# Optimization experiments

Measured on AMD Instinct MI355X. Metric: run time of the kernel, lower is better.

The kernel has to match this reference:

```python
import jax, jax.numpy as jnp
import numpy as np

B, C, H, W = 8, 512, 128, 128
WS = 8

def _proj(x, w, b):
    # 1x1 conv == channel GEMM: (B,C,H,W) x (Cout,Cin) -> (B,Cout,H,W)
    return jnp.einsum('bchw,oc->bohw', x, w) + b[None, :, None, None]

def _split_windows(x):
    # (B,C,H,W) -> (B*nH*nW, ws*ws, C)
    b, c, h, w = x.shape
    x = x.reshape(b, c, h // WS, WS, w // WS, WS)
    x = x.transpose(0, 2, 4, 3, 5, 1)
    return x.reshape(-1, WS * WS, c)

def _merge_windows(x, b, c, h, w):
    # (B*nH*nW, ws*ws, C) -> (B,C,H,W)
    x = x.reshape(b, h // WS, w // WS, WS, WS, c)
    x = x.transpose(0, 5, 1, 3, 2, 4)
    return x.reshape(b, c, h, w)

def setup_inputs() -> dict:
    key = jax.random.key(0)
    ks = jax.random.split(key, 9)
    s = 1.0 / np.sqrt(C)
    return {
        'x': jax.random.normal(ks[0], (B, C, H, W), jnp.float32),
        'wq': jax.random.normal(ks[1], (C, C), jnp.float32) * s,
        'bq': jnp.zeros((C,), jnp.float32),
        'wk': jax.random.normal(ks[2], (C, C), jnp.float32) * s,
        'bk': jnp.zeros((C,), jnp.float32),
        'wv': jax.random.normal(ks[3], (C, C), jnp.float32) * s,
        'bv': jnp.zeros((C,), jnp.float32),
        'wo': jax.random.normal(ks[4], (C, C), jnp.float32) * s,
        'bo': jnp.zeros((C,), jnp.float32),
    }

def reference(x, wq, bq, wk, bk, wv, bv, wo, bo):
    b, c, h, w = x.shape
    q = _split_windows(_proj(x, wq, bq))  # (nWin, ws*ws, C)
    k = _split_windows(_proj(x, wk, bk))
    v = _split_windows(_proj(x, wv, bv))
    attn = jnp.einsum('nqc,nkc->nqk', q, k) / jnp.sqrt(jnp.asarray(c, x.dtype))
    attn = jax.nn.softmax(attn, axis=-1)
    out = jnp.einsum('nqk,nkc->nqc', attn, v)
    out = _merge_windows(out, b, c, h, w)
    return _proj(out, wo, bo)
```

## Files before the change

### kernel.cpp

```cpp
#include <hip/hip_runtime.h>

typedef __attribute__((ext_vector_type(8))) short bf16x8;
typedef __attribute__((ext_vector_type(4))) float f32x4;

#define MFMA16(a, b, c) __builtin_amdgcn_mfma_f32_16x16x32_bf16((a), (b), (c), 0, 0, 0)

__device__ __forceinline__ float b2f(unsigned short u) {
  unsigned int v = ((unsigned int)u) << 16;
  return __builtin_bit_cast(float, v);
}
__device__ __forceinline__ unsigned short f2b(float f) {
  unsigned int u = __builtin_bit_cast(unsigned int, f);
  u += 0x7fffu + ((u >> 16) & 1u);
  return (unsigned short)(u >> 16);
}
__device__ __forceinline__ void gload16(const void* g, void* l) {
  __builtin_amdgcn_global_load_lds(
      (const __attribute__((address_space(1))) unsigned int*)g,
      (__attribute__((address_space(3))) unsigned int*)l, 16, 0, 0);
}

__global__ __launch_bounds__(256) void k_wconv(
    const float* __restrict__ src, unsigned short* __restrict__ dst) {
  const int i = (blockIdx.x * 256 + threadIdx.x) * 4;
  const float4 v = *(const float4*)(src + i);
  uint2 p;
  p.x = (unsigned int)f2b(v.x) | ((unsigned int)f2b(v.y) << 16);
  p.y = (unsigned int)f2b(v.z) | ((unsigned int)f2b(v.w) << 16);
  *(uint2*)(dst + i) = p;
}

__global__ __launch_bounds__(256) void k_wtrans(
    const float* __restrict__ in, unsigned short* __restrict__ out) {
  __shared__ unsigned short tile[64][72];
  const int r0 = blockIdx.x << 6, s0 = blockIdx.y << 6;
  const int t = threadIdx.x;
  {
    const int sl = t >> 3, rl = (t & 7) << 3;
#pragma unroll
    for (int pass = 0; pass < 2; ++pass) {
      const int s = sl + pass * 32;
      const float* src = in + (size_t)(s0 + s) * 512 + r0 + rl;
      const float4 f0 = ((const float4*)src)[0];
      const float4 f1 = ((const float4*)src)[1];
      tile[rl + 0][s] = f2b(f0.x);
      tile[rl + 1][s] = f2b(f0.y);
      tile[rl + 2][s] = f2b(f0.z);
      tile[rl + 3][s] = f2b(f0.w);
      tile[rl + 4][s] = f2b(f1.x);
      tile[rl + 5][s] = f2b(f1.y);
      tile[rl + 6][s] = f2b(f1.z);
      tile[rl + 7][s] = f2b(f1.w);
    }
  }
  __syncthreads();
  {
    const int rl = t >> 3, sl = (t & 7) << 3;
#pragma unroll
    for (int pass = 0; pass < 2; ++pass) {
      const int r = rl + pass * 32;
      uint4 v = *(const uint4*)&tile[r][sl];
      *(uint4*)(out + (size_t)(r0 + r) * 512 + s0 + sl) = v;
    }
  }
}

__global__ __launch_bounds__(256) void k_bvo(
    const float* __restrict__ wo, const float* __restrict__ bv,
    const float* __restrict__ bo, float* __restrict__ bvo) {
  const int o = blockIdx.x * 256 + threadIdx.x;
  float acc = bo[o];
  const float* row = wo + (size_t)o * 512;
  for (int j = 0; j < 512; ++j) acc += row[j] * bv[j];
  bvo[o] = acc;
}

__global__ __launch_bounds__(256) void k_ub(
    const float* __restrict__ wk, const float* __restrict__ bq,
    float* __restrict__ u) {
  const int c = blockIdx.x * 256 + threadIdx.x;
  float acc = 0.f;
  for (int o = 0; o < 512; ++o) acc += bq[o] * wk[(size_t)o * 512 + c];
  u[c] = acc;
}

__global__ __launch_bounds__(256) void k_transpose(
    const float* __restrict__ X, unsigned short* __restrict__ XT,
    unsigned short* __restrict__ XV) {
  const int bx = blockIdx.x;
  const int wt = bx & 1, ht = bx >> 1;
  const int c0 = blockIdx.y << 5;
  const int b = blockIdx.z;
  const int w0 = wt << 6, h0 = ht << 3;
  const int t = threadIdx.x;
  const int cg = t & 3, pg = t >> 2;
  const int wi = pg >> 3, hh = pg & 7;
  const int h = h0 + hh, w = w0 + wi * 8;
  const int cbase = c0 + cg * 8;

  const float* xsrc = X + (size_t)b * 8388608u + (size_t)cbase * 16384 +
                      (size_t)h * 128 + w;
  float f[8][8];
#pragma unroll
  for (int ci = 0; ci < 8; ++ci) {
    const float4 a0 = ((const float4*)(xsrc + (size_t)ci * 16384))[0];
    const float4 a1 = ((const float4*)(xsrc + (size_t)ci * 16384))[1];
    f[ci][0] = a0.x; f[ci][1] = a0.y; f[ci][2] = a0.z; f[ci][3] = a0.w;
    f[ci][4] = a1.x; f[ci][5] = a1.y; f[ci][6] = a1.z; f[ci][7] = a1.w;
  }

  unsigned short* xtdst =
      XT + (size_t)b * 8388608u + ((size_t)h * 128 + w) * 512 + cbase;
#pragma unroll
  for (int pi = 0; pi < 8; ++pi) {
    unsigned short o[8];
#pragma unroll
    for (int ci = 0; ci < 8; ++ci) o[ci] = f2b(f[ci][pi]);
    *(uint4*)(xtdst + (size_t)pi * 512) = *(const uint4*)o;
  }

  const int win = b * 256 + ht * 16 + wt * 8 + wi;
  unsigned short* xvdst =
      XV + (size_t)cbase * 131072 + (size_t)win * 64 + hh * 8;
#pragma unroll
  for (int ci = 0; ci < 8; ++ci) {
    unsigned short o[8];
#pragma unroll
    for (int pi = 0; pi < 8; ++pi) o[pi] = f2b(f[ci][pi]);
    *(uint4*)(xvdst + (size_t)ci * 131072) = *(const uint4*)o;
  }
}

template <int MODE>
__global__ __launch_bounds__(512, 2) void k_gemm256(
    const unsigned short* __restrict__ A, const unsigned short* __restrict__ B,
    const float* __restrict__ bias0, void* __restrict__ C0v) {
  __shared__ unsigned short lsA[4][256 * 32];
  __shared__ unsigned short lsB[4][256 * 32];
  const int bid = blockIdx.x;
  int mt, nt;
  if (MODE == 0) {
    const int work = ((bid & 7) << 7) + (bid >> 3);
    mt = work >> 1; nt = work & 1;
  } else if (MODE == 2) {
    const int work = ((bid & 7) << 7) + (bid >> 3);
    nt = work >> 1; mt = work & 1;
  } else {
    mt = bid & 1; nt = bid >> 1;
  }
  const int m0 = mt << 8, n0 = nt << 8;

  const int t = threadIdx.x;
  const int l = t & 63;
  const int lr = l & 15, lg = l >> 4;
  const int w = t >> 6;
  const int wr = w >> 2, wc = w & 3;
  const int ra = wr << 7, rb = wc << 6;
  const int srowS = t >> 2;
  const int scolS = (t & 3) << 3;

  f32x4 acc[8][4];
#pragma unroll
  for (int i = 0; i < 8; ++i)
#pragma unroll
    for (int j = 0; j < 4; ++j) acc[i][j] = f32x4{0.f, 0.f, 0.f, 0.f};

  auto stage = [&](int kt) {
    const int buf = kt & 3, k0 = kt << 5;
#pragma unroll
    for (int hh = 0; hh < 2; ++hh) {
      gload16(A + (size_t)(m0 + srowS + hh * 128) * 512 + k0 + scolS,
              &lsA[buf][(srowS + hh * 128) * 32 + scolS]);
      gload16(B + (size_t)(n0 + srowS + hh * 128) * 512 + k0 + scolS,
              &lsB[buf][(srowS + hh * 128) * 32 + scolS]);
    }
  };
  auto compute = [&](int kt) {
    const int buf = kt & 3;
    bf16x8 af[8], bfv[4];
#pragma unroll
    for (int i = 0; i < 8; ++i)
      af[i] = *(const bf16x8*)&lsA[buf][(ra + i * 16 + lr) * 32 + lg * 8];
#pragma unroll
    for (int j = 0; j < 4; ++j)
      bfv[j] = *(const bf16x8*)&lsB[buf][(rb + j * 16 + lr) * 32 + lg * 8];
    __builtin_amdgcn_s_setprio(1);
#pragma unroll
    for (int i = 0; i < 8; ++i)
#pragma unroll
      for (int j = 0; j < 4; ++j)
        acc[i][j] = MFMA16(af[i], bfv[j], acc[i][j]);
    __builtin_amdgcn_s_setprio(0);
  };

  stage(0); stage(1); stage(2);

#define GITER(kt, vm)                                        \
  asm volatile("s_waitcnt vmcnt(" #vm ")" ::: "memory");     \
  __builtin_amdgcn_s_barrier();                              \
  __builtin_amdgcn_sched_barrier(0);                         \
  if ((kt) + 3 < 16) stage((kt) + 3);                        \
  compute(kt);                                               \
  __builtin_amdgcn_sched_barrier(0);                         \
  __builtin_amdgcn_s_barrier();

  GITER(0, 8)  GITER(1, 8)  GITER(2, 8)  GITER(3, 8)
  GITER(4, 8)  GITER(5, 8)  GITER(6, 8)  GITER(7, 8)
  GITER(8, 8)  GITER(9, 8)  GITER(10, 8) GITER(11, 8)
  GITER(12, 8) GITER(13, 8) GITER(14, 4) GITER(15, 0)
#undef GITER

#pragma unroll
  for (int i = 0; i < 8; ++i) {
    const int cmb = m0 + ra + i * 16 + lg * 4;
#pragma unroll
    for (int j = 0; j < 4; ++j) {
      const int cn = n0 + rb + j * 16 + lr;
      const float bn = (MODE == 0) ? bias0[cn] : 0.f;
#pragma unroll
      for (int r = 0; r < 4; ++r) {
        const int cm = cmb + r;
        if (MODE == 0) {
          ((unsigned short*)C0v)[(size_t)cm * 512 + cn] = f2b(acc[i][j][r] + bn);
        } else if (MODE == 2) {
          const float val = acc[i][j][r] + bias0[cm];
          const int bb = cn >> 14, p = cn & 16383;
          ((float*)C0v)[(size_t)bb * 8388608 + (size_t)cm * 16384 + p] = val;
        } else {
          ((unsigned short*)C0v)[(size_t)cm * 512 + cn] = f2b(acc[i][j][r]);
        }
      }
    }
  }
}

__global__ __launch_bounds__(256) void k_attn(
    const unsigned short* __restrict__ Q, const unsigned short* __restrict__ XT,
    const unsigned short* __restrict__ XV, unsigned short* __restrict__ Y) {
  __shared__ unsigned short P_lds[4][64][72];
  const int t = threadIdx.x, w = t >> 6, l = t & 63;
  const int lr = l & 15, lg = l >> 4;
  const int grp = ((blockIdx.x & 7) << 6) + (blockIdx.x >> 3);
  const int win = grp * 4 + w;
  const int b = win >> 8, th = (win >> 4) & 15, tw = win & 15;
  const size_t p_base = (size_t)b * 16384 + (size_t)th * 1024 + (size_t)tw * 8;
  const size_t rowpix = p_base + (size_t)(lr >> 3) * 128 + (lr & 7);
  const unsigned short* qbase = Q + rowpix * 512;
  const unsigned short* kbase = XT + rowpix * 512;

  f32x4 acc[4][4];
#pragma unroll
  for (int i = 0; i < 4; ++i)
#pragma unroll
    for (int j = 0; j < 4; ++j) acc[i][j] = f32x4{0.f, 0.f, 0.f, 0.f};

  bf16x8 kp[2][4], qp[2][4];
#pragma unroll
  for (int pp = 0; pp < 2; ++pp) {
    const int co = pp * 32 + lg * 8;
#pragma unroll
    for (int i = 0; i < 4; ++i) {
      kp[pp][i] = *(const bf16x8*)(kbase + (size_t)i * 131072 + co);
      qp[pp][i] = *(const bf16x8*)(qbase + (size_t)i * 131072 + co);
    }
  }
#pragma unroll
  for (int cs = 0; cs < 16; ++cs) {
    const int cb = cs & 1;
    __builtin_amdgcn_s_setprio(1);
#pragma unroll
    for (int mt = 0; mt < 4; ++mt)
#pragma unroll
      for (int qt = 0; qt < 4; ++qt)
        acc[mt][qt] = MFMA16(kp[cb][mt], qp[cb][qt], acc[mt][qt]);
    __builtin_amdgcn_s_setprio(0);
    if (cs + 2 < 16) {
      const int co = (cs + 2) * 32 + lg * 8;
#pragma unroll
      for (int i = 0; i < 4; ++i) {
        kp[cb][i] = *(const bf16x8*)(kbase + (size_t)i * 131072 + co);
        qp[cb][i] = *(const bf16x8*)(qbase + (size_t)i * 131072 + co);
      }
    }
  }

  const float scale = 0.044194173824159216f;
#pragma unroll
  for (int qt = 0; qt < 4; ++qt) {
    float pv[4][4];
    float mx = -3.0e38f;
#pragma unroll
    for (int mt = 0; mt < 4; ++mt)
#pragma unroll
      for (int j = 0; j < 4; ++j) {
        const float s = acc[mt][qt][j] * scale;
        pv[mt][j] = s;
        mx = fmaxf(mx, s);
      }
    mx = fmaxf(mx, __shfl_xor(mx, 16));
    mx = fmaxf(mx, __shfl_xor(mx, 32));
    float sum = 0.f;
#pragma unroll
    for (int mt = 0; mt < 4; ++mt)
#pragma unroll
      for (int j = 0; j < 4; ++j) {
        const float e = __expf(pv[mt][j] - mx);
        pv[mt][j] = e;
        sum += e;
      }
    sum += __shfl_xor(sum, 16);
    sum += __shfl_xor(sum, 32);
    const float inv = 1.f / sum;
#pragma unroll
    for (int mt = 0; mt < 4; ++mt)
#pragma unroll
      for (int j = 0; j < 4; j += 2) {
        const unsigned int pk =
            (unsigned int)f2b(pv[mt][j] * inv) |
            ((unsigned int)f2b(pv[mt][j + 1] * inv) << 16);
        *(unsigned int*)&P_lds[w][qt * 16 + lr][mt * 16 + lg * 4 + j] = pk;
      }
  }

  bf16x8 pa0[4], pa1[4];
#pragma unroll
  for (int qt = 0; qt < 4; ++qt) {
    pa0[qt] = *(const bf16x8*)&P_lds[w][qt * 16 + lr][lg * 8];
    pa1[qt] = *(const bf16x8*)&P_lds[w][qt * 16 + lr][32 + lg * 8];
  }
  const unsigned short* vbase =
      XV + (size_t)lr * 131072 + (size_t)win * 64 + lg * 8;
  unsigned short* ystore =
      Y + (p_base + (size_t)(lg >> 1) * 128 + ((lg & 1) << 2)) * 512 + lr;

  bf16x8 v0p[2], v1p[2];
#pragma unroll
  for (int pp = 0; pp < 2; ++pp) {
    const unsigned short* vp = vbase + (size_t)pp * (16 * 131072);
    v0p[pp] = *(const bf16x8*)vp;
    v1p[pp] = *(const bf16x8*)(vp + 32);
  }
#pragma unroll
  for (int nt = 0; nt < 32; ++nt) {
    const int cb = nt & 1;
    f32x4 o[4];
    __builtin_amdgcn_s_setprio(1);
#pragma unroll
    for (int qt = 0; qt < 4; ++qt) {
      o[qt] = f32x4{0.f, 0.f, 0.f, 0.f};
      o[qt] = MFMA16(pa0[qt], v0p[cb], o[qt]);
      o[qt] = MFMA16(pa1[qt], v1p[cb], o[qt]);
    }
    __builtin_amdgcn_s_setprio(0);
    if (nt + 2 < 32) {
      const unsigned short* vp = vbase + (size_t)(nt + 2) * (16 * 131072);
      v0p[cb] = *(const bf16x8*)vp;
      v1p[cb] = *(const bf16x8*)(vp + 32);
    }
#pragma unroll
    for (int qt = 0; qt < 4; ++qt)
#pragma unroll
      for (int r = 0; r < 4; ++r)
        ystore[(size_t)qt * 131072 + r * 512 + nt * 16] = f2b(o[qt][r]);
  }
}

extern "C" void kernel_launch(void* const* d_in, const int* in_sizes, int n_in,
                              void* d_out, int out_size, void* d_ws,
                              size_t ws_size, hipStream_t stream) {
  (void)in_sizes; (void)n_in; (void)out_size;
  const float* x = (const float*)d_in[0];
  const float* wq = (const float*)d_in[1];
  const float* bq = (const float*)d_in[2];
  const float* wk = (const float*)d_in[3];
  const float* bk = (const float*)d_in[4];
  const float* wv = (const float*)d_in[5];
  const float* bv = (const float*)d_in[6];
  const float* wo = (const float*)d_in[7];
  const float* bo = (const float*)d_in[8];
  (void)bk;

  const size_t NEED = (size_t)(2097152 + 3 * 67108864) * 2;
  if (ws_size < NEED) return;

  unsigned short* wb = (unsigned short*)d_ws;
  unsigned short* wqT = wb;
  unsigned short* wkT = wb + 262144;
  unsigned short* wvT = wb + 524288;
  unsigned short* wo_b = wb + 786432;
  unsigned short* wvo = wb + 1048576;
  float* bvo = (float*)(wb + 1310720);
  float* ub = (float*)(wb + 1311744);
  unsigned short* Bqk = wb + 1572864;
  unsigned short* xT = wb + 2097152;
  unsigned short* xV = xT + 67108864;
  unsigned short* Ybuf = xV + 67108864;
  unsigned short* Tq = (unsigned short*)d_out;

  k_wtrans<<<dim3(8, 8), 256, 0, stream>>>(wq, wqT);
  k_wtrans<<<dim3(8, 8), 256, 0, stream>>>(wk, wkT);
  k_wtrans<<<dim3(8, 8), 256, 0, stream>>>(wv, wvT);
  k_wconv<<<256, 256, 0, stream>>>(wo, wo_b);
  k_gemm256<3><<<4, 512, 0, stream>>>(wkT, wqT, nullptr, Bqk);
  k_gemm256<3><<<4, 512, 0, stream>>>(wo_b, wvT, nullptr, wvo);
  k_ub<<<2, 256, 0, stream>>>(wk, bq, ub);
  k_bvo<<<2, 256, 0, stream>>>(wo, bv, bo, bvo);
  k_transpose<<<dim3(32, 16, 8), 256, 0, stream>>>(x, xT, xV);
  k_gemm256<0><<<1024, 512, 0, stream>>>(xT, Bqk, ub, Tq);
  k_attn<<<512, 256, 0, stream>>>(Tq, xT, xV, Ybuf);
  k_gemm256<2><<<1024, 512, 0, stream>>>(wvo, Ybuf, bvo, d_out);
}
```

Before: 583.5 us.

## Shrink GEMM tiles to 128x128 and merge small prep kernels

The 256x256 GEMM kernel (512 threads, 8 waves) becomes a 128x128 kernel (256 threads, 4 waves), with grid counts scaled up and the tile-swizzle mapping adjusted. The three weight-transpose launches are merged into one launch using blockIdx.z, and the two bias kernels are merged into one. Smaller tiles give more blocks and less LDS per block, which may raise occupancy, but they lower operand reuse per tile and add global/LDS traffic. The merged prep kernels remove some launch overhead.

```diff
diff --git a/kernel.cpp b/kernel.cpp
--- a/kernel.cpp
+++ b/kernel.cpp
@@ -30,9 +30,13 @@
   *(uint2*)(dst + i) = p;
 }
 
-__global__ __launch_bounds__(256) void k_wtrans(
-    const float* __restrict__ in, unsigned short* __restrict__ out) {
+__global__ __launch_bounds__(256) void k_wtrans3(
+    const float* __restrict__ wq, const float* __restrict__ wk,
+    const float* __restrict__ wv, unsigned short* __restrict__ outbase) {
   __shared__ unsigned short tile[64][72];
+  const int z = blockIdx.z;
+  const float* in = (z == 0) ? wq : (z == 1) ? wk : wv;
+  unsigned short* out = outbase + (size_t)z * 262144u;
   const int r0 = blockIdx.x << 6, s0 = blockIdx.y << 6;
   const int t = threadIdx.x;
   {
@@ -65,23 +69,24 @@
   }
 }
 
-__global__ __launch_bounds__(256) void k_bvo(
+__global__ __launch_bounds__(256) void k_bias(
     const float* __restrict__ wo, const float* __restrict__ bv,
-    const float* __restrict__ bo, float* __restrict__ bvo) {
-  const int o = blockIdx.x * 256 + threadIdx.x;
-  float acc = bo[o];
-  const float* row = wo + (size_t)o * 512;
-  for (int j = 0; j < 512; ++j) acc += row[j] * bv[j];
-  bvo[o] = acc;
-}
-
-__global__ __launch_bounds__(256) void k_ub(
-    const float* __restrict__ wk, const float* __restrict__ bq,
+    const float* __restrict__ bo, const float* __restrict__ wk,
+    const float* __restrict__ bq, float* __restrict__ bvo,
     float* __restrict__ u) {
-  const int c = blockIdx.x * 256 + threadIdx.x;
-  float acc = 0.f;
-  for (int o = 0; o < 512; ++o) acc += bq[o] * wk[(size_t)o * 512 + c];
-  u[c] = acc;
+  const int bid = blockIdx.x;
+  if (bid < 2) {
+    const int o = bid * 256 + threadIdx.x;
+    float acc = bo[o];
+    const float* row = wo + (size_t)o * 512;
+    for (int j = 0; j < 512; ++j) acc += row[j] * bv[j];
+    bvo[o] = acc;
+  } else {
+    const int c = (bid - 2) * 256 + threadIdx.x;
+    float acc = 0.f;
+    for (int o = 0; o < 512; ++o) acc += bq[o] * wk[(size_t)o * 512 + c];
+    u[c] = acc;
+  }
 }
 
 __global__ __launch_bounds__(256) void k_transpose(
@@ -132,36 +137,36 @@
 }
 
 template <int MODE>
-__global__ __launch_bounds__(512, 2) void k_gemm256(
+__global__ __launch_bounds__(256, 2) void k_gemm128(
     const unsigned short* __restrict__ A, const unsigned short* __restrict__ B,
     const float* __restrict__ bias0, void* __restrict__ C0v) {
-  __shared__ unsigned short lsA[4][256 * 32];
-  __shared__ unsigned short lsB[4][256 * 32];
+  __shared__ unsigned short lsA[4][128 * 32];
+  __shared__ unsigned short lsB[4][128 * 32];
   const int bid = blockIdx.x;
   int mt, nt;
   if (MODE == 0) {
-    const int work = ((bid & 7) << 7) + (bid >> 3);
-    mt = work >> 1; nt = work & 1;
+    const int work = ((bid & 7) << 9) + (bid >> 3);
+    mt = work >> 2; nt = work & 3;
   } else if (MODE == 2) {
-    const int work = ((bid & 7) << 7) + (bid >> 3);
-    nt = work >> 1; mt = work & 1;
+    const int work = ((bid & 7) << 9) + (bid >> 3);
+    nt = work >> 2; mt = work & 3;
   } else {
-    mt = bid & 1; nt = bid >> 1;
-  }
-  const int m0 = mt << 8, n0 = nt << 8;
+    mt = bid & 3; nt = bid >> 2;
+  }
+  const int m0 = mt << 7, n0 = nt << 7;
 
   const int t = threadIdx.x;
   const int l = t & 63;
   const int lr = l & 15, lg = l >> 4;
   const int w = t >> 6;
-  const int wr = w >> 2, wc = w & 3;
-  const int ra = wr << 7, rb = wc << 6;
+  const int wr = w >> 1, wc = w & 1;
+  const int ra = wr << 6, rb = wc << 6;
   const int srowS = t >> 2;
   const int scolS = (t & 3) << 3;
 
-  f32x4 acc[8][4];
-#pragma unroll
-  for (int i = 0; i < 8; ++i)
+  f32x4 acc[4][4];
+#pragma unroll
+  for (int i = 0; i < 4; ++i)
 #pragma unroll
     for (int j = 0; j < 4; ++j) acc[i][j] = f32x4{0.f, 0.f, 0.f, 0.f};
 
@@ -169,24 +174,24 @@
     const int buf = kt & 3, k0 = kt << 5;
 #pragma unroll
     for (int hh = 0; hh < 2; ++hh) {
-      gload16(A + (size_t)(m0 + srowS + hh * 128) * 512 + k0 + scolS,
-              &lsA[buf][(srowS + hh * 128) * 32 + scolS]);
-      gload16(B + (size_t)(n0 + srowS + hh * 128) * 512 + k0 + scolS,
-              &lsB[buf][(srowS + hh * 128) * 32 + scolS]);
+      gload16(A + (size_t)(m0 + srowS + hh * 64) * 512 + k0 + scolS,
+              &lsA[buf][(srowS + hh * 64) * 32 + scolS]);
+      gload16(B + (size_t)(n0 + srowS + hh * 64) * 512 + k0 + scolS,
+              &lsB[buf][(srowS + hh * 64) * 32 + scolS]);
     }
   };
   auto compute = [&](int kt) {
     const int buf = kt & 3;
-    bf16x8 af[8], bfv[4];
-#pragma unroll
-    for (int i = 0; i < 8; ++i)
+    bf16x8 af[4], bfv[4];
+#pragma unroll
+    for (int i = 0; i < 4; ++i)
       af[i] = *(const bf16x8*)&lsA[buf][(ra + i * 16 + lr) * 32 + lg * 8];
 #pragma unroll
     for (int j = 0; j < 4; ++j)
       bfv[j] = *(const bf16x8*)&lsB[buf][(rb + j * 16 + lr) * 32 + lg * 8];
     __builtin_amdgcn_s_setprio(1);
 #pragma unroll
-    for (int i = 0; i < 8; ++i)
+    for (int i = 0; i < 4; ++i)
 #pragma unroll
       for (int j = 0; j < 4; ++j)
         acc[i][j] = MFMA16(af[i], bfv[j], acc[i][j]);
@@ -211,7 +216,7 @@
 #undef GITER
 
 #pragma unroll
-  for (int i = 0; i < 8; ++i) {
+  for (int i = 0; i < 4; ++i) {
     const int cmb = m0 + ra + i * 16 + lg * 4;
 #pragma unroll
     for (int j = 0; j < 4; ++j) {
@@ -385,7 +390,6 @@
 
   unsigned short* wb = (unsigned short*)d_ws;
   unsigned short* wqT = wb;
-  unsigned short* wkT = wb + 262144;
   unsigned short* wvT = wb + 524288;
   unsigned short* wo_b = wb + 786432;
   unsigned short* wvo = wb + 1048576;
@@ -397,16 +401,13 @@
   unsigned short* Ybuf = xV + 67108864;
   unsigned short* Tq = (unsigned short*)d_out;
 
-  k_wtrans<<<dim3(8, 8), 256, 0, stream>>>(wq, wqT);
-  k_wtrans<<<dim3(8, 8), 256, 0, stream>>>(wk, wkT);
-  k_wtrans<<<dim3(8, 8), 256, 0, stream>>>(wv, wvT);
+  k_wtrans3<<<dim3(8, 8, 3), 256, 0, stream>>>(wq, wk, wv, wqT);
   k_wconv<<<256, 256, 0, stream>>>(wo, wo_b);
-  k_gemm256<3><<<4, 512, 0, stream>>>(wkT, wqT, nullptr, Bqk);
-  k_gemm256<3><<<4, 512, 0, stream>>>(wo_b, wvT, nullptr, wvo);
-  k_ub<<<2, 256, 0, stream>>>(wk, bq, ub);
-  k_bvo<<<2, 256, 0, stream>>>(wo, bv, bo, bvo);
+  k_bias<<<4, 256, 0, stream>>>(wo, bv, bo, wk, bq, bvo, ub);
+  k_gemm128<3><<<16, 256, 0, stream>>>(wqT + 262144, wqT, nullptr, Bqk);
+  k_gemm128<3><<<16, 256, 0, stream>>>(wo_b, wvT, nullptr, wvo);
   k_transpose<<<dim3(32, 16, 8), 256, 0, stream>>>(x, xT, xV);
-  k_gemm256<0><<<1024, 512, 0, stream>>>(xT, Bqk, ub, Tq);
+  k_gemm128<0><<<4096, 256, 0, stream>>>(xT, Bqk, ub, Tq);
   k_attn<<<512, 256, 0, stream>>>(Tq, xT, xV, Ybuf);
-  k_gemm256<2><<<1024, 512, 0, stream>>>(wvo, Ybuf, bvo, d_out);
-}
+  k_gemm128<2><<<4096, 256, 0, stream>>>(wvo, Ybuf, bvo, d_out);
+}
```

Result: slower. 612.7 us (+5.0%).
